# Kernel optimization log

Hardware: AMD Instinct MI355X
Metric: run time of the kernel (lower is better)

## Reference

```python
import jax, jax.numpy as jnp
import numpy as np

C_IN = 512
OUT_CH = 256  # query/key gate channels
DIM = 64      # squeeze/extraction rank


def setup_inputs() -> dict:
    key = jax.random.key(0)
    ks = jax.random.split(key, 11)
    b, c, h, w = 16, C_IN, 64, 64

    def winit(k, o, i):
        # torch Conv2d default init: U(-s, s), s = 1/sqrt(fan_in)
        s = 1.0 / np.sqrt(i)
        return jax.random.uniform(k, (o, i), jnp.float32, -s, s)

    return {
        "x": jax.random.normal(ks[0], (b, c, h, w), jnp.float32),
        "Wq": winit(ks[1], OUT_CH, C_IN), "bq": winit(ks[2], OUT_CH, C_IN)[:, 0],
        "Wk": winit(ks[3], OUT_CH, C_IN), "bk": winit(ks[4], OUT_CH, C_IN)[:, 0],
        "Wv": winit(ks[5], C_IN, C_IN),   "bv": winit(ks[6], C_IN, C_IN)[:, 0],
        "Ws": winit(ks[7], DIM, C_IN),    "bs": winit(ks[8], DIM, C_IN)[:, 0],
        "We": winit(ks[9], DIM, C_IN),    "be": winit(ks[10], DIM, C_IN)[:, 0],
    }


def reference(x, Wq, bq, Wk, bk, Wv, bv, Ws, bs, We, be):
    b, c, h, w = x.shape
    n = h * w
    xf = x.reshape(b, c, n)  # [b, 512, n] (1x1 conv == matmul over channels)

    Q = jnp.einsum('oc,bcn->bon', Wq, xf) + bq[:, None]   # [b, 256, n]
    K = jnp.einsum('oc,bcn->bon', Wk, xf) + bk[:, None]   # [b, 256, n]
    gate = jax.nn.sigmoid(jnp.mean(Q * K, axis=1, keepdims=True))  # [b, 1, n]

    V = jnp.einsum('oc,bcn->bon', Wv, xf) + bv[:, None]   # [b, 512, n]
    V_dw = V * gate                                        # [b, 512, n]

    Qs = jnp.einsum('oc,bcn->bon', Ws, xf) + bs[:, None]   # [b, 64, n]
    Ke = jnp.einsum('oc,bcn->bon', We, xf) + be[:, None]   # [b, 64, n]

    energy = jnp.einsum('bcn,bdn->bcd', V_dw, Qs)           # [b, 512, 64]
    attention = jax.nn.softmax(energy, axis=-1)
    Vout = jnp.einsum('bcd,bdn->bcn', attention, Ke)        # [b, 512, n]

    return x + Vout.reshape(b, c, h, w)
```

## Files before the change

kernel.cpp:

```cpp
#include <hip/hip_runtime.h>

#define BATCH 16
#define CIN 512
#define NPIX 4096

typedef __attribute__((ext_vector_type(8))) short bf16x8;
typedef __attribute__((ext_vector_type(4))) float f32x4;

#define MFMA(a,b,c) __builtin_amdgcn_mfma_f32_16x16x32_bf16((a),(b),(c),0,0,0)

#define GLOAD(g, l) __builtin_amdgcn_global_load_lds( \
    (const __attribute__((address_space(1))) unsigned int*)(g), \
    (__attribute__((address_space(3))) unsigned int*)(l), 16, 0, 0)

union PK  { short s[8]; bf16x8 v; };
union PK4 { short s[4]; uint2 u; };

__device__ __forceinline__ unsigned short bf16_rne(float f){
  unsigned u = __float_as_uint(f);
  return (unsigned short)((u + 0x7fffu + ((u >> 16) & 1u)) >> 16);
}
__device__ __forceinline__ void f32_split(float f, short &h, short &l){
  unsigned short hu = bf16_rne(f);
  h = (short)hu;
  float fh = __uint_as_float((unsigned)hu << 16);
  l = (short)bf16_rne(f - fh);
}
__device__ __forceinline__ void split8(float4 a, float4 b, bf16x8 &h, bf16x8 &l){
  float vv[8] = {a.x,a.y,a.z,a.w,b.x,b.y,b.z,b.w};
  PK ph, pl;
  #pragma unroll
  for (int z=0;z<8;z++){ short hh,ll; f32_split(vv[z],hh,ll); ph.s[z]=hh; pl.s[z]=ll; }
  h = ph.v; l = pl.v;
}

__device__ __forceinline__ int offBig(int row, int k){
  int s = k >> 3;
  s = (s & ~7) | ((s ^ row) & 7);
  return row*512 + s*8 + (k & 7);
}

__global__ __launch_bounds__(256)
void k_convw(const float* __restrict__ Wq, const float* __restrict__ bq,
             const float* __restrict__ Wk, const float* __restrict__ bk,
             const float* __restrict__ Ws, const float* __restrict__ bs,
             const float* __restrict__ We, const float* __restrict__ be,
             short* __restrict__ WALL, short* __restrict__ WLOT,
             float* __restrict__ BG, float* __restrict__ BSE){
  int t = blockIdx.x*256 + threadIdx.x;
  if (t < 640*512){
    int r = t >> 9, k = t & 511;
    float v = (r < 512) ? ((r & 1) ? Wk[(r>>1)*512 + k] : Wq[(r>>1)*512 + k])
            : (r < 576) ? Ws[(r-512)*512 + k] : We[(r-576)*512 + k];
    short h, l; f32_split(v, h, l);
    int kt = k >> 5, lc = (k >> 3) & 3, e = k & 7;
    int pc = lc ^ (r & 3);
    WALL[((size_t)kt*640 + r)*32 + pc*8 + e] = h;
    if (r >= 512 && r < 576){
      int rlo = r - 512;
      WLOT[((size_t)kt*64 + rlo)*32 + (lc ^ (rlo & 3))*8 + e] = l;
    }
  }
  if (t < 512) BG[t] = (t & 1) ? bk[t>>1] : bq[t>>1];
  if (t < 128) BSE[t] = (t < 64) ? bs[t] : be[t-64];
}

__global__ __launch_bounds__(512, 2)
void k_front(const float* __restrict__ x, const short* __restrict__ WALL,
             const short* __restrict__ WLOT, const float* __restrict__ BG,
             const float* __restrict__ BSE,
             float* __restrict__ QSG, short* __restrict__ KET, float* __restrict__ S){
  __shared__ __align__(16) short AB[2][640*32];
  __shared__ __align__(16) short LO[2][64*32];
  __shared__ __align__(16) short XS[64*512];
  __shared__ float QKf[512];
  __shared__ float GF[64];
  int nt = blockIdx.x, b = blockIdx.y;
  int n0 = nt*64;
  int tid = threadIdx.x, w = tid>>6, lane = tid&63;
  int lr = lane&15, lk = (lane>>4)<<3;
  int cg = lane>>4;

  {
    const char* src = (const char*)WALL;
    #pragma unroll
    for (int i=0;i<5;i++){
      int slot = i*8 + w;
      GLOAD(src + slot*1024 + lane*16, ((char*)&AB[0][0]) + slot*1024);
    }
    if (w < 4)
      GLOAD((const char*)WLOT + w*1024 + lane*16, ((char*)&LO[0][0]) + w*1024);
  }

  {
    const float* xp = x + ((size_t)b*CIN + tid)*NPIX + n0;
    float4 vv[16];
    #pragma unroll
    for (int i=0;i<16;i++) vv[i] = *(const float4*)(xp + i*4);
    #pragma unroll
    for (int i=0;i<16;i++){
      float f[4] = {vv[i].x, vv[i].y, vv[i].z, vv[i].w};
      #pragma unroll
      for (int u=0;u<4;u++)
        XS[offBig(i*4+u, tid)] = (short)bf16_rne(f[u]);
    }
  }

  f32x4 acc[5][4] = {};
  int rowBase = w*80;

  for (int kt=0; kt<16; kt++){
    int cur = kt & 1;
    __syncthreads();
    if (kt < 15){
      const char* src = (const char*)WALL + (size_t)(kt+1)*40960;
      #pragma unroll
      for (int i=0;i<5;i++){
        int slot = i*8 + w;
        GLOAD(src + slot*1024 + lane*16, ((char*)&AB[cur^1][0]) + slot*1024);
      }
      if (w < 4)
        GLOAD((const char*)WLOT + (size_t)(kt+1)*4096 + w*1024 + lane*16,
              ((char*)&LO[cur^1][0]) + w*1024);
    }
    bf16x8 bb[4];
    #pragma unroll
    for (int j=0;j<4;j++)
      bb[j] = *(const bf16x8*)&XS[offBig(j*16+lr, kt*32+lk)];
    int swz = ((cg ^ (lr & 3)) << 3);
    #pragma unroll
    for (int r=0;r<5;r++){
      int rowL = rowBase + r*16 + lr;
      bf16x8 a = *(const bf16x8*)&AB[cur][rowL*32 + swz];
      #pragma unroll
      for (int j=0;j<4;j++) acc[r][j] = MFMA(a, bb[j], acc[r][j]);
      int F = w*5 + r;
      if (F >= 32 && F < 36){
        int rowLo = F*16 - 512 + lr;
        bf16x8 alo = *(const bf16x8*)&LO[cur][rowLo*32 + swz];
        #pragma unroll
        for (int j=0;j<4;j++) acc[r][j] = MFMA(alo, bb[j], acc[r][j]);
      }
    }
  }

  int rq = (lane>>4)<<2;
  {
    float p[4] = {0.f,0.f,0.f,0.f};
    #pragma unroll
    for (int r=0;r<5;r++){
      int F = w*5 + r;
      if (F < 32){
        f32x4 bg = *(const f32x4*)&BG[F*16 + rq];
        #pragma unroll
        for (int j=0;j<4;j++){
          f32x4 a4 = acc[r][j];
          p[j] += (a4[0]+bg[0])*(a4[1]+bg[1]) + (a4[2]+bg[2])*(a4[3]+bg[3]);
        }
      }
    }
    #pragma unroll
    for (int j=0;j<4;j++){ p[j] += __shfl_xor(p[j],16); p[j] += __shfl_xor(p[j],32); }
    if (lane < 16){
      #pragma unroll
      for (int j=0;j<4;j++) QKf[w*64 + j*16 + lane] = p[j];
    }
  }
  __syncthreads();
  if (tid < 64){
    float s = 0.f;
    #pragma unroll
    for (int ww=0;ww<8;ww++) s += QKf[ww*64 + tid];
    GF[tid] = 1.f/(1.f + __expf(-s*(1.f/256.f)));
  }
  __syncthreads();

  #pragma unroll
  for (int r=0;r<5;r++){
    int F = w*5 + r;
    if (F >= 32 && F < 36){
      int row0 = F*16 - 512 + rq;
      f32x4 bs4 = *(const f32x4*)&BSE[row0];
      float srow[4] = {0.f,0.f,0.f,0.f};
      #pragma unroll
      for (int j=0;j<4;j++){
        int nl = j*16 + lr;
        float g = GF[nl];
        int n = n0 + nl;
        #pragma unroll
        for (int q=0;q<4;q++){
          float v = (acc[r][j][q] + bs4[q]) * g;
          QSG[((size_t)(b*64) + row0 + q)*NPIX + n] = v;
          srow[q] += v;
        }
      }
      #pragma unroll
      for (int q=0;q<4;q++){
        float v = srow[q];
        v += __shfl_xor(v,1); v += __shfl_xor(v,2);
        v += __shfl_xor(v,4); v += __shfl_xor(v,8);
        if (lr == 0) atomicAdd(&S[b*64 + row0 + q], v);
      }
    } else if (F >= 36){
      int d0 = F*16 - 576 + rq;
      f32x4 be4 = *(const f32x4*)&BSE[64 + d0];
      #pragma unroll
      for (int j=0;j<4;j++){
        int n = n0 + j*16 + lr;
        PK4 pk;
        #pragma unroll
        for (int q=0;q<4;q++) pk.s[q] = (short)bf16_rne(acc[r][j][q] + be4[q]);
        *(uint2*)&KET[((size_t)(b*NPIX) + n)*64 + d0] = pk.u;
      }
    }
  }
}

__global__ __launch_bounds__(512)
void k_M(const float* __restrict__ x, const float* __restrict__ QSG,
         float* __restrict__ M){
  int slab = blockIdx.x, b = blockIdx.y;
  int tid = threadIdx.x, w = tid>>6, lane = tid&63;
  int lr = lane&15, lk8 = (lane>>4)<<3;
  f32x4 acc[4][4] = {};
  for (int kt=0; kt<8; kt++){
    int noff = slab*256 + kt*32 + lk8;
    bf16x8 bh[4], bl[4];
    #pragma unroll
    for (int j=0;j<4;j++){
      const float* qp = QSG + ((size_t)(b*64) + j*16 + lr)*NPIX + noff;
      split8(*(const float4*)qp, *(const float4*)(qp+4), bh[j], bl[j]);
    }
    #pragma unroll
    for (int r=0;r<4;r++){
      const float* xp = x + ((size_t)(b*CIN) + w*64 + r*16 + lr)*NPIX + noff;
      bf16x8 ah, al;
      split8(*(const float4*)xp, *(const float4*)(xp+4), ah, al);
      #pragma unroll
      for (int j=0;j<4;j++){
        acc[r][j] = MFMA(al, bh[j], acc[r][j]);
        acc[r][j] = MFMA(ah, bl[j], acc[r][j]);
        acc[r][j] = MFMA(ah, bh[j], acc[r][j]);
      }
    }
  }
  int rq = (lane>>4)<<2;
  #pragma unroll
  for (int r=0;r<4;r++)
    #pragma unroll
    for (int j=0;j<4;j++)
      #pragma unroll
      for (int q=0;q<4;q++)
        atomicAdd(&M[((size_t)(b*CIN) + w*64 + r*16 + rq + q)*64 + j*16 + lr], acc[r][j][q]);
}

__global__ __launch_bounds__(256)
void k_energy(const float* __restrict__ Wv, const float* __restrict__ bv,
              const float* __restrict__ M, const float* __restrict__ S,
              float* __restrict__ EN){
  __shared__ __align__(16) float ML[128*68];
  int cch = blockIdx.x, b = blockIdx.y;
  int tid = threadIdx.x;
  int d4 = tid & 15, ci = tid >> 4;
  f32x4 acc[2] = {};
  for (int kt=0; kt<4; kt++){
    __syncthreads();
    for (int i = tid; i < 2048; i += 256){
      int k = i >> 4, c4 = (i & 15) * 4;
      *(float4*)&ML[k*68 + c4] = *(const float4*)&M[((size_t)(b*CIN) + kt*128 + k)*64 + c4];
    }
    __syncthreads();
    #pragma unroll
    for (int m=0;m<2;m++){
      int c = cch*32 + ci + 16*m;
      const float* wvp = Wv + (size_t)c*512 + kt*128;
      for (int k4=0;k4<32;k4++){
        float4 wv4 = *(const float4*)(wvp + k4*4);
        f32x4 m0 = *(const f32x4*)&ML[(k4*4+0)*68 + d4*4];
        f32x4 m1 = *(const f32x4*)&ML[(k4*4+1)*68 + d4*4];
        f32x4 m2 = *(const f32x4*)&ML[(k4*4+2)*68 + d4*4];
        f32x4 m3 = *(const f32x4*)&ML[(k4*4+3)*68 + d4*4];
        acc[m] += m0*wv4.x + m1*wv4.y + m2*wv4.z + m3*wv4.w;
      }
    }
  }
  f32x4 s4 = *(const f32x4*)&S[b*64 + d4*4];
  #pragma unroll
  for (int m=0;m<2;m++){
    int c = cch*32 + ci + 16*m;
    f32x4 r = acc[m] + s4*bv[c];
    *(f32x4*)&EN[((size_t)(b*CIN) + c)*64 + d4*4] = r;
  }
}

__global__ __launch_bounds__(256)
void k_softmax(const float* __restrict__ EN, short* __restrict__ ATT){
  int row = blockIdx.x*4 + (threadIdx.x>>6);
  int lane = threadIdx.x & 63;
  float v = EN[(size_t)row*64 + lane];
  float m = v;
  #pragma unroll
  for (int s=1;s<64;s<<=1) m = fmaxf(m, __shfl_xor(m, s));
  float e = __expf(v - m);
  float sum = e;
  #pragma unroll
  for (int s=1;s<64;s<<=1) sum += __shfl_xor(sum, s);
  ATT[(size_t)row*64 + lane] = (short)bf16_rne(e / sum);
}

__global__ __launch_bounds__(512)
void k_out(const float* __restrict__ x, const short* __restrict__ ATT,
           const short* __restrict__ KET, float* __restrict__ out){
  int nt = blockIdx.x, b = blockIdx.y;
  int n0 = nt*64;
  int tid = threadIdx.x, w = tid>>6, lane = tid&63;
  int lr = lane&15, lk = (lane>>4)<<3;
  f32x4 acc[4][4] = {};
  #pragma unroll
  for (int kt=0; kt<2; kt++){
    bf16x8 bb[4];
    #pragma unroll
    for (int j=0;j<4;j++)
      bb[j] = *(const bf16x8*)&KET[((size_t)(b*NPIX) + n0 + j*16 + lr)*64 + kt*32 + lk];
    #pragma unroll
    for (int r=0;r<4;r++){
      bf16x8 a = *(const bf16x8*)&ATT[((size_t)(b*CIN) + w*64 + r*16 + lr)*64 + kt*32 + lk];
      #pragma unroll
      for (int j=0;j<4;j++)
        acc[r][j] = MFMA(a, bb[j], acc[r][j]);
    }
  }
  int rq = (lane>>4)<<2;
  #pragma unroll
  for (int r=0;r<4;r++)
    #pragma unroll
    for (int j=0;j<4;j++){
      int col = n0 + j*16 + lr;
      #pragma unroll
      for (int q=0;q<4;q++){
        size_t idx = ((size_t)(b*CIN) + w*64 + r*16 + rq + q)*NPIX + col;
        out[idx] = x[idx] + acc[r][j][q];
      }
    }
}

extern "C" void kernel_launch(void* const* d_in, const int* in_sizes, int n_in,
                              void* d_out, int out_size, void* d_ws, size_t ws_size,
                              hipStream_t stream){
  const float* x   = (const float*)d_in[0];
  const float* Wq  = (const float*)d_in[1];
  const float* bq  = (const float*)d_in[2];
  const float* Wk  = (const float*)d_in[3];
  const float* bk  = (const float*)d_in[4];
  const float* Wv  = (const float*)d_in[5];
  const float* bv  = (const float*)d_in[6];
  const float* Wsq = (const float*)d_in[7];
  const float* bsq = (const float*)d_in[8];
  const float* We  = (const float*)d_in[9];
  const float* be  = (const float*)d_in[10];
  float* out = (float*)d_out;

  char* wsb = (char*)d_ws;
  size_t off = 0;
  auto alloc = [&](size_t bytes)->void*{
    void* p = wsb + off; off += (bytes + 255) & ~(size_t)255; return p;
  };
  short* WALL = (short*)alloc((size_t)640*512*2);
  short* WLOT = (short*)alloc((size_t)64*512*2);
  float* BG   = (float*)alloc(512*4);
  float* BSE  = (float*)alloc(128*4);
  float* QSG  = (float*)alloc((size_t)BATCH*64*NPIX*4);
  short* KET  = (short*)alloc((size_t)BATCH*NPIX*64*2);
  float* Mb   = (float*)alloc((size_t)BATCH*512*64*4);
  float* Sb   = (float*)alloc((size_t)BATCH*64*4);
  float* EN   = (float*)alloc((size_t)BATCH*512*64*4);
  short* ATT  = (short*)alloc((size_t)BATCH*512*64*2);

  hipMemsetAsync(Mb, 0, (size_t)BATCH*512*64*4, stream);
  hipMemsetAsync(Sb, 0, (size_t)BATCH*64*4, stream);

  k_convw  <<<1280, 256, 0, stream>>>(Wq,bq,Wk,bk,Wsq,bsq,We,be, WALL,WLOT,BG,BSE);
  k_front  <<<dim3(64,16), 512, 0, stream>>>(x, WALL, WLOT, BG, BSE, QSG, KET, Sb);
  k_M      <<<dim3(16,16), 512, 0, stream>>>(x, QSG, Mb);
  k_energy <<<dim3(16,16), 256, 0, stream>>>(Wv, bv, Mb, Sb, EN);
  k_softmax<<<2048, 256, 0, stream>>>(EN, ATT);
  k_out    <<<dim3(64,16), 512, 0, stream>>>(x, ATT, KET, out);
}
```

Baseline: 278.8 us.

## Split front kernel into bf16 transpose stage and weight-from-global GEMM

Splits the front kernel in two. A new staging kernel converts x to bf16 in a transposed, swizzled layout held in a workspace buffer. The GEMM kernel then bulk-loads that tile into LDS with async global-to-LDS copies and reads the weights straight from global memory or cache, instead of double-buffering them through LDS. This cuts LDS usage, which may raise occupancy, and removes per-step barriers. The cost is an extra launch plus roughly 64MB of bf16 intermediate traffic written and read back, and uncoalesced weight loads that depend on cache hits.

```diff
diff --git a/kernel.cpp b/kernel.cpp
--- a/kernel.cpp
+++ b/kernel.cpp
@@ -65,16 +65,46 @@
   if (t < 128) BSE[t] = (t < 64) ? bs[t] : be[t-64];
 }
 
-__global__ __launch_bounds__(512, 2)
-void k_front(const float* __restrict__ x, const short* __restrict__ WALL,
-             const short* __restrict__ WLOT, const float* __restrict__ BG,
-             const float* __restrict__ BSE,
-             float* __restrict__ QSG, short* __restrict__ KET, float* __restrict__ S){
-  __shared__ __align__(16) short AB[2][640*32];
-  __shared__ __align__(16) short LO[2][64*32];
+__global__ __launch_bounds__(256)
+void k_stage(const float* __restrict__ x, short* __restrict__ XT){
+  __shared__ float XF[64*65];
+  int cb = blockIdx.x, nb = blockIdx.y, b = blockIdx.z;
+  int tid = threadIdx.x;
+  {
+    int cc = tid >> 2, ni = (tid & 3) * 16;
+    const float* xp = x + ((size_t)(b*CIN + cb*64 + cc))*NPIX + nb*64 + ni;
+    #pragma unroll
+    for (int u=0;u<16;u+=4){
+      float4 v = *(const float4*)(xp + u);
+      XF[cc*65 + ni+u+0] = v.x; XF[cc*65 + ni+u+1] = v.y;
+      XF[cc*65 + ni+u+2] = v.z; XF[cc*65 + ni+u+3] = v.w;
+    }
+  }
+  __syncthreads();
+  {
+    int nn = tid & 63, cg = (tid >> 6) * 16;
+    PK c0, c1;
+    #pragma unroll
+    for (int i=0;i<8;i++) c0.s[i] = (short)bf16_rne(XF[(cg+i)*65 + nn]);
+    #pragma unroll
+    for (int i=0;i<8;i++) c1.s[i] = (short)bf16_rne(XF[(cg+8+i)*65 + nn]);
+    short* dst = XT + ((size_t)(b*64 + nb))*64*512;
+    int ch0 = cb*8 + (cg>>3), ch1 = ch0 + 1;
+    int s0 = (ch0 & ~7) | ((ch0 ^ nn) & 7);
+    int s1 = (ch1 & ~7) | ((ch1 ^ nn) & 7);
+    *(bf16x8*)&dst[nn*512 + s0*8] = c0.v;
+    *(bf16x8*)&dst[nn*512 + s1*8] = c1.v;
+  }
+}
+
+__global__ __launch_bounds__(512)
+void k_gemm(const short* __restrict__ XT, const short* __restrict__ WALL,
+            const short* __restrict__ WLOT, const float* __restrict__ BG,
+            const float* __restrict__ BSE,
+            float* __restrict__ QSG, short* __restrict__ KET, float* __restrict__ S){
   __shared__ __align__(16) short XS[64*512];
-  __shared__ float QKf[512];
-  __shared__ float GF[64];
+  float* QKf = (float*)XS;
+  float* GF  = ((float*)XS) + 512;
   int nt = blockIdx.x, b = blockIdx.y;
   int n0 = nt*64;
   int tid = threadIdx.x, w = tid>>6, lane = tid&63;
@@ -82,67 +112,39 @@
   int cg = lane>>4;
 
   {
-    const char* src = (const char*)WALL;
-    #pragma unroll
-    for (int i=0;i<5;i++){
-      int slot = i*8 + w;
-      GLOAD(src + slot*1024 + lane*16, ((char*)&AB[0][0]) + slot*1024);
-    }
-    if (w < 4)
-      GLOAD((const char*)WLOT + w*1024 + lane*16, ((char*)&LO[0][0]) + w*1024);
-  }
-
-  {
-    const float* xp = x + ((size_t)b*CIN + tid)*NPIX + n0;
-    float4 vv[16];
-    #pragma unroll
-    for (int i=0;i<16;i++) vv[i] = *(const float4*)(xp + i*4);
-    #pragma unroll
-    for (int i=0;i<16;i++){
-      float f[4] = {vv[i].x, vv[i].y, vv[i].z, vv[i].w};
-      #pragma unroll
-      for (int u=0;u<4;u++)
-        XS[offBig(i*4+u, tid)] = (short)bf16_rne(f[u]);
-    }
-  }
+    const char* src = (const char*)(XT + ((size_t)(b*64 + nt))*64*512);
+    char* dstbase = (char*)XS;
+    #pragma unroll
+    for (int i=0;i<8;i++)
+      GLOAD(src + i*8192 + tid*16, dstbase + i*8192 + (tid & ~63)*16);
+  }
+  __syncthreads();
 
   f32x4 acc[5][4] = {};
   int rowBase = w*80;
+  int swz = ((cg ^ (lr & 3)) << 3);
 
   for (int kt=0; kt<16; kt++){
-    int cur = kt & 1;
-    __syncthreads();
-    if (kt < 15){
-      const char* src = (const char*)WALL + (size_t)(kt+1)*40960;
-      #pragma unroll
-      for (int i=0;i<5;i++){
-        int slot = i*8 + w;
-        GLOAD(src + slot*1024 + lane*16, ((char*)&AB[cur^1][0]) + slot*1024);
-      }
-      if (w < 4)
-        GLOAD((const char*)WLOT + (size_t)(kt+1)*4096 + w*1024 + lane*16,
-              ((char*)&LO[cur^1][0]) + w*1024);
-    }
     bf16x8 bb[4];
     #pragma unroll
     for (int j=0;j<4;j++)
       bb[j] = *(const bf16x8*)&XS[offBig(j*16+lr, kt*32+lk)];
-    int swz = ((cg ^ (lr & 3)) << 3);
+    const short* wk = WALL + (size_t)kt*640*32;
     #pragma unroll
     for (int r=0;r<5;r++){
       int rowL = rowBase + r*16 + lr;
-      bf16x8 a = *(const bf16x8*)&AB[cur][rowL*32 + swz];
+      bf16x8 a = *(const bf16x8*)&wk[rowL*32 + swz];
       #pragma unroll
       for (int j=0;j<4;j++) acc[r][j] = MFMA(a, bb[j], acc[r][j]);
       int F = w*5 + r;
       if (F >= 32 && F < 36){
-        int rowLo = F*16 - 512 + lr;
-        bf16x8 alo = *(const bf16x8*)&LO[cur][rowLo*32 + swz];
+        bf16x8 alo = *(const bf16x8*)&WLOT[(size_t)kt*64*32 + (F*16-512+lr)*32 + swz];
         #pragma unroll
         for (int j=0;j<4;j++) acc[r][j] = MFMA(alo, bb[j], acc[r][j]);
       }
     }
   }
+  __syncthreads();
 
   int rq = (lane>>4)<<2;
   {
@@ -369,6 +371,7 @@
   short* WLOT = (short*)alloc((size_t)64*512*2);
   float* BG   = (float*)alloc(512*4);
   float* BSE  = (float*)alloc(128*4);
+  short* XT   = (short*)alloc((size_t)BATCH*NPIX*512*2);
   float* QSG  = (float*)alloc((size_t)BATCH*64*NPIX*4);
   short* KET  = (short*)alloc((size_t)BATCH*NPIX*64*2);
   float* Mb   = (float*)alloc((size_t)BATCH*512*64*4);
@@ -380,7 +383,8 @@
   hipMemsetAsync(Sb, 0, (size_t)BATCH*64*4, stream);
 
   k_convw  <<<1280, 256, 0, stream>>>(Wq,bq,Wk,bk,Wsq,bsq,We,be, WALL,WLOT,BG,BSE);
-  k_front  <<<dim3(64,16), 512, 0, stream>>>(x, WALL, WLOT, BG, BSE, QSG, KET, Sb);
+  k_stage  <<<dim3(8,64,16), 256, 0, stream>>>(x, XT);
+  k_gemm   <<<dim3(64,16), 512, 0, stream>>>(XT, WALL, WLOT, BG, BSE, QSG, KET, Sb);
   k_M      <<<dim3(16,16), 512, 0, stream>>>(x, QSG, Mb);
   k_energy <<<dim3(16,16), 256, 0, stream>>>(Wv, bv, Mb, Sb, EN);
   k_softmax<<<2048, 256, 0, stream>>>(EN, ATT);
```

Result: slower. 310.9 us (+11.5%).
